# Optimization experiments

Measured on AMD Instinct MI355X. Metric: run time of the kernel, lower is better.

The kernel has to match this reference:

```python
import jax, jax.numpy as jnp
import numpy as np

T, B, IN_DIM, HID, ACT = 512, 256, 256, 256, 16


def _dense_params(key, din, dout, scale=0.02):
    kw, _ = jax.random.split(key)
    return jax.random.normal(kw, (din, dout), jnp.float32) * scale, jnp.zeros((dout,), jnp.float32)


def setup_inputs() -> dict:
    key = jax.random.key(0)
    ks = jax.random.split(key, 12)
    x = jax.random.normal(ks[0], (T, B, IN_DIM), jnp.float32)
    dones = jax.random.bernoulli(ks[1], 0.05, (T, B))
    h0_c = jnp.zeros((B, HID), jnp.float32)
    h0_h = jnp.zeros((B, HID), jnp.float32)
    W_embed, b_embed = _dense_params(ks[2], IN_DIM, HID)
    # OptimizedLSTMCell: fused gate projections, gate order (i, f, g, o)
    Wi = jax.random.normal(ks[3], (HID, 4 * HID), jnp.float32) * 0.02
    Wh = jax.random.normal(ks[4], (HID, 4 * HID), jnp.float32) * 0.02
    b_lstm = jnp.zeros((4 * HID,), jnp.float32)
    Wa1, ba1 = _dense_params(ks[5], HID, HID // 2)
    Wa2, ba2 = _dense_params(ks[6], HID // 2, HID // 2)
    Wa3, ba3 = _dense_params(ks[7], HID // 2, ACT, scale=0.01)
    Wc1, bc1 = _dense_params(ks[8], HID, HID // 2)
    Wc2, bc2 = _dense_params(ks[9], HID // 2, HID // 2)
    Wc3, bc3 = _dense_params(ks[10], HID // 2, 1)
    return dict(x=x, dones=dones, h0_c=h0_c, h0_h=h0_h,
                W_embed=W_embed, b_embed=b_embed, Wi=Wi, Wh=Wh, b_lstm=b_lstm,
                Wa1=Wa1, ba1=ba1, Wa2=Wa2, ba2=ba2, Wa3=Wa3, ba3=ba3,
                Wc1=Wc1, bc1=bc1, Wc2=Wc2, bc2=bc2, Wc3=Wc3, bc3=bc3)


def reference(x, dones, h0_c, h0_h, W_embed, b_embed, Wi, Wh, b_lstm,
              Wa1, ba1, Wa2, ba2, Wa3, ba3, Wc1, bc1, Wc2, bc2, Wc3, bc3):
    # embed (note: source overwrites first Dense; effective embed is one Dense+relu)
    embed = jax.nn.relu(jnp.einsum('tbi,ih->tbh', x, W_embed) + b_embed)

    def step(carry, inp):
        c, h = carry
        xt, rt = inp  # xt: [B, HID], rt: [B] bool
        m = rt[:, None]
        c = jnp.where(m, 0.0, c)  # reset_carry is zeros (initialize_carry)
        h = jnp.where(m, 0.0, h)
        z = xt @ Wi + h @ Wh + b_lstm  # [B, 4*HID]
        i, f, g, o = jnp.split(z, 4, axis=-1)
        c_new = jax.nn.sigmoid(f) * c + jax.nn.sigmoid(i) * jnp.tanh(g)
        h_new = jax.nn.sigmoid(o) * jnp.tanh(c_new)
        return (c_new, h_new), h_new

    (c_fin, h_fin), hs = jax.lax.scan(step, (h0_c, h0_h), (embed, dones))

    a = jnp.tanh(jnp.einsum('tbh,hk->tbk', hs, Wa1) + ba1)
    a = jnp.tanh(a @ Wa2 + ba2)
    logits = a @ Wa3 + ba3  # [T, B, ACT]

    v = jnp.tanh(jnp.einsum('tbh,hk->tbk', hs, Wc1) + bc1)
    v = jnp.tanh(v @ Wc2 + bc2)
    value = jnp.squeeze(v @ Wc3 + bc3, axis=-1)  # [T, B]

    return c_fin, h_fin, logits, value
```

## Files before the change

kernel.cpp:

```cpp
#include <hip/hip_runtime.h>
#include <stdint.h>


typedef short v8s __attribute__((ext_vector_type(8)));
typedef float v4f __attribute__((ext_vector_type(4)));

#define DEV static __device__ __forceinline__
#define DT_THRESH 4096

DEV float b2f(unsigned short h) {
    union { unsigned int u; float f; } v; v.u = ((unsigned int)h) << 16; return v.f;
}
DEV unsigned short f2b(float f) {
    union { float f; unsigned int u; } v; v.f = f;
    unsigned int u = v.u;
    return (unsigned short)((u + 0x7fffu + ((u >> 16) & 1u)) >> 16);
}
DEV float sigf(float x) {
    x = fminf(fmaxf(x, -30.f), 30.f);
    return 1.f / (1.f + __expf(-x));
}
DEV float tanh_(float x) {
    x = fminf(fmaxf(x, -15.f), 15.f);
    float e = __expf(-2.f * x);
    return (1.f - e) / (1.f + e);
}

__global__ __launch_bounds__(1024) void dones_k(const void* __restrict__ raw,
                                                int* __restrict__ dst,
                                                int* __restrict__ dt) {
    __shared__ int bad_int, bad_bf;
    int tid = threadIdx.x;
    if (tid == 0) { bad_int = 0; bad_bf = 0; dt[0] = 0; }
    __syncthreads();
    const unsigned int* w = (const unsigned int*)raw;
    int li = 0, lb = 0;
    for (int i = tid; i < 32768; i += 1024) {
        unsigned int v = w[i];
        if (v > 1u) li = 1;
        unsigned int h0 = v & 0xffffu, h1 = v >> 16;
        if ((h0 != 0u && h0 != 0x3f80u) || (h1 != 0u && h1 != 0x3f80u)) lb = 1;
    }
    if (li) atomicOr(&bad_int, 1);
    if (lb) atomicOr(&bad_bf, 1);
    __syncthreads();
    int mode = (!bad_int) ? 0 : ((!bad_bf) ? 1 : 2);
    for (int e = tid; e < 131072; e += 1024) {
        int v;
        if (mode == 0)      v = (((const int*)raw)[e] != 0);
        else if (mode == 1) v = (((const unsigned short*)raw)[e] != 0);
        else                v = (((const unsigned char*)raw)[e] != 0);
        dst[e] = v;
    }
}

__global__ __launch_bounds__(256) void detect_k(const unsigned short* __restrict__ xr,
                                                int* __restrict__ dt) {
    int tid = blockIdx.x * 256 + threadIdx.x;
    int cnt = 0;
    for (int i = tid; i < (1 << 24); i += 16384) {
        unsigned int e = (xr[i] >> 7) & 0xffu;
        cnt += (e >= 140u);
    }
    for (int o = 32; o; o >>= 1) cnt += __shfl_down(cnt, o);
    if ((threadIdx.x & 63) == 0 && cnt) atomicAdd(dt, cnt);
}

__global__ __launch_bounds__(256) void cvt_x_k(const void* __restrict__ xr,
                                               unsigned short* __restrict__ xb,
                                               const int* __restrict__ dt) {
    int fp32i = dt[0] > DT_THRESH;
    long i4 = (long)blockIdx.x * 256 + threadIdx.x;
    if (fp32i) {
        float4 v = ((const float4*)xr)[i4];
        uint2 p;
        p.x = (unsigned int)f2b(v.x) | ((unsigned int)f2b(v.y) << 16);
        p.y = (unsigned int)f2b(v.z) | ((unsigned int)f2b(v.w) << 16);
        ((uint2*)xb)[i4] = p;
    } else {
        ((uint2*)xb)[i4] = ((const uint2*)xr)[i4];
    }
}

struct TransArgs {
    const void* src[9];
    unsigned short* dst[9];
    int R[9];
    int C[9];
    int prefix[10];
    int total;
};

__global__ __launch_bounds__(256) void trans_kernel(TransArgs a, const int* __restrict__ dt) {
    int fp32i = dt[0] > DT_THRESH;
    int id = blockIdx.x * 256 + threadIdx.x;
    if (id >= a.total) return;
    int m = 0;
#pragma unroll
    for (int k = 0; k < 9; k++)
        if (id >= a.prefix[k + 1]) m = k + 1;
    int e = id - a.prefix[m];
    int C = a.C[m];
    int r = e / C, c = e % C;
    unsigned short v;
    if (fp32i) v = f2b(((const float*)a.src[m])[e]);
    else       v = ((const unsigned short*)a.src[m])[e];
    a.dst[m][c * a.R[m] + r] = v;
}

template <int TN, int ACT, int OM>
__global__ __launch_bounds__(256) void gemm_k(const unsigned short* __restrict__ A,
                                              const unsigned short* __restrict__ BT,
                                              const unsigned short* __restrict__ bias,
                                              void* __restrict__ Cout, long coff,
                                              const int* __restrict__ dtf,
                                              int N, int K) {
    __shared__ unsigned short As[128][40];
    __shared__ unsigned short Bs[TN][40];
    const int tid = threadIdx.x;
    const int l = tid & 63, w = tid >> 6;
    const long m0 = (long)blockIdx.x * 128;
    const int n0 = blockIdx.y * TN;
    constexpr int NRT = (TN == 128) ? 4 : 2;
    constexpr int NCT = (TN == 128) ? 4 : 1;
    int fp32o = (OM == 1) ? (dtf[0] > DT_THRESH) : 0;

    v4f acc[NRT][NCT];
    for (int i = 0; i < NRT; i++)
        for (int j = 0; j < NCT; j++) acc[i][j] = v4f{0.f, 0.f, 0.f, 0.f};

    for (int kc = 0; kc < K; kc += 32) {
        {
            int row = tid >> 1, part = tid & 1;
            const uint4* src = (const uint4*)(A + (m0 + row) * K + kc + part * 16);
            uint4 v0 = src[0], v1 = src[1];
            *(uint4*)&As[row][part * 16] = v0;
            *(uint4*)&As[row][part * 16 + 8] = v1;
        }
        if (TN == 128) {
            int row = tid >> 1, part = tid & 1;
            const uint4* src = (const uint4*)(BT + (long)(n0 + row) * K + kc + part * 16);
            uint4 v0 = src[0], v1 = src[1];
            *(uint4*)&Bs[row][part * 16] = v0;
            *(uint4*)&Bs[row][part * 16 + 8] = v1;
        } else if (tid < 32) {
            int row = tid >> 1, part = tid & 1;
            const uint4* src = (const uint4*)(BT + (long)(n0 + row) * K + kc + part * 16);
            uint4 v0 = src[0], v1 = src[1];
            *(uint4*)&Bs[row][part * 16] = v0;
            *(uint4*)&Bs[row][part * 16 + 8] = v1;
        }
        __syncthreads();

        v8s af[NRT], bf[NCT];
#pragma unroll
        for (int i = 0; i < NRT; i++) {
            int rt = (TN == 128) ? ((w >> 1) * 4 + i) : (w * 2 + i);
            af[i] = *(const v8s*)&As[rt * 16 + (l & 15)][(l >> 4) * 8];
        }
#pragma unroll
        for (int j = 0; j < NCT; j++) {
            int ct = (TN == 128) ? ((w & 1) * 4 + j) : 0;
            bf[j] = *(const v8s*)&Bs[ct * 16 + (l & 15)][(l >> 4) * 8];
        }
#pragma unroll
        for (int i = 0; i < NRT; i++)
#pragma unroll
            for (int j = 0; j < NCT; j++)
                acc[i][j] = __builtin_amdgcn_mfma_f32_16x16x32_bf16(af[i], bf[j], acc[i][j], 0, 0, 0);
        __syncthreads();
    }

#pragma unroll
    for (int j = 0; j < NCT; j++) {
        int ct = (TN == 128) ? ((w & 1) * 4 + j) : 0;
        int col = ct * 16 + (l & 15);
        float bv = b2f(bias[n0 + col]);
#pragma unroll
        for (int i = 0; i < NRT; i++) {
            int rt = (TN == 128) ? ((w >> 1) * 4 + i) : (w * 2 + i);
#pragma unroll
            for (int q = 0; q < 4; q++) {
                long row = m0 + rt * 16 + (l >> 4) * 4 + q;
                float v = acc[i][j][q] + bv;
                if (ACT == 1) v = fmaxf(v, 0.f);
                if (ACT == 2) v = tanh_(v);
                long idx = coff + row * (long)N + n0 + col;
                if (OM == 1 && fp32o) ((float*)Cout)[idx] = v;
                else ((unsigned short*)Cout)[idx] = f2b(v);
            }
        }
    }
}

#define HB_WORDS 65536

__global__ __launch_bounds__(64) void lstm_k(const unsigned short* __restrict__ xz,
                                             const int* __restrict__ dones,
                                             const void* __restrict__ h0c,
                                             const void* __restrict__ h0h,
                                             const unsigned short* __restrict__ WhT,
                                             unsigned int* __restrict__ hb,
                                             unsigned short* __restrict__ hs,
                                             void* __restrict__ outv,
                                             const int* __restrict__ dtf) {
    __shared__ unsigned short Whs[64][264];
    __shared__ unsigned short hlds[16][264];
    __shared__ unsigned short xzs[16][72];
    __shared__ int dns[16];

    const int l = threadIdx.x;
    const int cluster = blockIdx.x & 15;
    const int rank = blockIdx.x >> 4;
    const int bt = cluster * 16;
    const int m = l & 15;
    const int qq = l >> 4;
    const int hc = rank * 16 + m;
    const int fp32o = dtf[0] > DT_THRESH;
    const int meven = ((m & 1) == 0);

    {
        int zc = qq * 256 + rank * 16 + m;
        const unsigned short* srcp = WhT + (long)zc * 256;
#pragma unroll
        for (int k8 = 0; k8 < 32; k8++) {
            uint4 v = *(const uint4*)(srcp + k8 * 8);
            *(uint4*)&Whs[l][k8 * 8] = v;
        }
    }
    __syncthreads();

    float c[4], hn[4];
#pragma unroll
    for (int q = 0; q < 4; q++) {
        int row = qq * 4 + q;
        long idx = (long)(bt + row) * 256 + hc;
        c[q] = fp32o ? ((const float*)h0c)[idx] : b2f(((const unsigned short*)h0c)[idx]);
        float h0 = fp32o ? ((const float*)h0h)[idx] : b2f(((const unsigned short*)h0h)[idx]);
        unsigned short hbits = f2b(h0);
        __hip_atomic_store(&hb[(size_t)cluster * 4096 + row * 256 + hc],
                           (unsigned int)hbits,
                           __ATOMIC_RELAXED, __HIP_MEMORY_SCOPE_AGENT);
        hn[q] = 0.f;
    }

    int dead = 0;
    unsigned int va[64];

    for (int t = 0; t < 512; t++) {
        const unsigned int tag = (unsigned int)t;
        const unsigned int* rb = hb + (size_t)(t & 1) * HB_WORDS + (size_t)cluster * 4096;

        if (l < 16) dns[l] = dones[t * 256 + bt + l];
        {
            int row = l >> 2, g = l & 3;
            const uint4* src = (const uint4*)(xz + ((long)(t * 256 + bt + row)) * 1024 + g * 256 + rank * 16);
            uint4 v0 = src[0], v1 = src[1];
            *(uint4*)&xzs[row][g * 16] = v0;
            *(uint4*)&xzs[row][g * 16 + 8] = v1;
        }

        if (!dead) {
            int guard = 0;
            while (true) {
#pragma unroll
                for (int i = 0; i < 64; i++)
                    va[i] = __hip_atomic_load(&rb[i * 64 + l],
                                              __ATOMIC_RELAXED, __HIP_MEMORY_SCOPE_AGENT);
                unsigned int okl = 1u;
#pragma unroll
                for (int i = 0; i < 64; i++) okl &= ((va[i] >> 16) == tag) ? 1u : 0u;
                if (__ballot(okl != 0u) == ~0ull) break;
                if (++guard > (1 << 13)) { dead = 1; break; }
            }
        }

#pragma unroll
        for (int i = 0; i < 64; i++)
            hlds[i >> 2][(i & 3) * 64 + l] = (unsigned short)(va[i] & 0xffffu);
        __syncthreads();

        int dnA = dns[m];
        v4f acc[4];
#pragma unroll
        for (int g = 0; g < 4; g++) acc[g] = v4f{0.f, 0.f, 0.f, 0.f};
#pragma unroll
        for (int ks = 0; ks < 8; ks++) {
            v8s a = *(const v8s*)&hlds[m][ks * 32 + qq * 8];
            if (dnA) a = v8s{0, 0, 0, 0, 0, 0, 0, 0};
#pragma unroll
            for (int g = 0; g < 4; g++) {
                v8s b = *(const v8s*)&Whs[g * 16 + m][ks * 32 + qq * 8];
                acc[g] = __builtin_amdgcn_mfma_f32_16x16x32_bf16(a, b, acc[g], 0, 0, 0);
            }
        }

        unsigned int* wb = hb + (size_t)((t + 1) & 1) * HB_WORDS + (size_t)cluster * 4096;
#pragma unroll
        for (int q = 0; q < 4; q++) {
            int row = qq * 4 + q;
            float zi = acc[0][q] + b2f(xzs[row][0 + m]);
            float zf = acc[1][q] + b2f(xzs[row][16 + m]);
            float zg = acc[2][q] + b2f(xzs[row][32 + m]);
            float zo = acc[3][q] + b2f(xzs[row][48 + m]);
            float cm = dns[row] ? 0.f : c[q];
            float cn = sigf(zf) * cm + sigf(zi) * tanh_(zg);
            float h = sigf(zo) * tanh_(cn);
            c[q] = cn;
            hn[q] = h;
            unsigned short hbits = f2b(h);
            __hip_atomic_store(&wb[row * 256 + hc],
                               (((unsigned int)(t + 1)) << 16) | (unsigned int)hbits,
                               __ATOMIC_RELAXED, __HIP_MEMORY_SCOPE_AGENT);
            unsigned int pr = (unsigned int)__shfl_xor((int)hbits, 1);
            if (meven) {
                unsigned int wv = (unsigned int)hbits | (pr << 16);
                ((unsigned int*)hs)[((long)(t * 256 + bt + row)) * 128 + rank * 8 + (m >> 1)] = wv;
            }
        }
        __syncthreads();
    }

#pragma unroll
    for (int q = 0; q < 4; q++) {
        int row = qq * 4 + q;
        long i1 = (long)(bt + row) * 256 + hc;
        long i2 = 65536 + i1;
        if (fp32o) {
            ((float*)outv)[i1] = c[q];
            ((float*)outv)[i2] = hn[q];
        } else {
            ((unsigned short*)outv)[i1] = f2b(c[q]);
            ((unsigned short*)outv)[i2] = f2b(hn[q]);
        }
    }
}

__global__ __launch_bounds__(256) void value_k(const unsigned short* __restrict__ V2,
                                               const unsigned short* __restrict__ Wc3T,
                                               const unsigned short* __restrict__ bc3,
                                               void* __restrict__ outv,
                                               const int* __restrict__ dtf) {
    int tid = threadIdx.x;
    int l = tid & 63, w = tid >> 6;
    int fp32o = dtf[0] > DT_THRESH;
    long row = (long)blockIdx.x * 32 + w * 8 + (l >> 3);
    int sub = l & 7;
    const unsigned short* vp = V2 + row * 128 + sub * 16;
    float s = 0.f;
#pragma unroll
    for (int j = 0; j < 16; j++) s += b2f(vp[j]) * b2f(Wc3T[sub * 16 + j]);
    s += __shfl_xor(s, 1);
    s += __shfl_xor(s, 2);
    s += __shfl_xor(s, 4);
    if (sub == 0) {
        float v = s + b2f(bc3[0]);
        if (fp32o) ((float*)outv)[2228224 + row] = v;
        else ((unsigned short*)outv)[2228224 + row] = f2b(v);
    }
}

extern "C" void kernel_launch(void* const* d_in, const int* in_sizes, int n_in,
                              void* d_out, int out_size, void* d_ws, size_t ws_size,
                              hipStream_t stream) {
    const void* x             = d_in[0];
    const void* dones_raw     = d_in[1];
    const void* h0c           = d_in[2];
    const void* h0h           = d_in[3];
    const void* We  = d_in[4];
    const unsigned short* be  = (const unsigned short*)d_in[5];
    const void* Wi  = d_in[6];
    const void* Wh  = d_in[7];
    const unsigned short* bl  = (const unsigned short*)d_in[8];
    const void* Wa1 = d_in[9];
    const unsigned short* ba1 = (const unsigned short*)d_in[10];
    const void* Wa2 = d_in[11];
    const unsigned short* ba2 = (const unsigned short*)d_in[12];
    const void* Wa3 = d_in[13];
    const unsigned short* ba3 = (const unsigned short*)d_in[14];
    const void* Wc1 = d_in[15];
    const unsigned short* bc1 = (const unsigned short*)d_in[16];
    const void* Wc2 = d_in[17];
    const unsigned short* bc2 = (const unsigned short*)d_in[18];
    const void* Wc3 = d_in[19];
    const unsigned short* bc3 = (const unsigned short*)d_in[20];
    char* ws = (char*)d_ws;

    unsigned short* WeT  = (unsigned short*)(ws + 0);
    unsigned short* WiT  = (unsigned short*)(ws + 131072);
    unsigned short* WhT  = (unsigned short*)(ws + 655360);
    unsigned short* Wa1T = (unsigned short*)(ws + 1179648);
    unsigned short* Wa2T = (unsigned short*)(ws + 1245184);
    unsigned short* Wa3T = (unsigned short*)(ws + 1277952);
    unsigned short* Wc1T = (unsigned short*)(ws + 1282048);
    unsigned short* Wc2T = (unsigned short*)(ws + 1347584);
    unsigned short* Wc3T = (unsigned short*)(ws + 1380352);
    int*            DT   = (int*)(ws + 1380608);
    unsigned int*   HB   = (unsigned int*)(ws + 1380672);
    int*            DN   = (int*)(ws + 1904960);
    unsigned short* XB   = (unsigned short*)(ws + 2429248);
    unsigned short* E    = (unsigned short*)(ws + 69538112);
    unsigned short* XZ   = (unsigned short*)(ws + 136646976);
    unsigned short* HS   = (unsigned short*)(ws + 405082432);
    unsigned short* H1   = XB;
    unsigned short* H2   = XB + 16777216;

    TransArgs ta;
    {
        const void* srcs[9] = {We, Wi, Wh, Wa1, Wa2, Wa3, Wc1, Wc2, Wc3};
        unsigned short* dsts[9] = {WeT, WiT, WhT, Wa1T, Wa2T, Wa3T, Wc1T, Wc2T, Wc3T};
        int Rs[9] = {256, 256, 256, 256, 128, 128, 256, 128, 128};
        int Cs[9] = {256, 1024, 1024, 128, 128, 16, 128, 128, 1};
        int p = 0;
        for (int i = 0; i < 9; i++) {
            ta.src[i] = srcs[i];
            ta.dst[i] = dsts[i];
            ta.R[i] = Rs[i];
            ta.C[i] = Cs[i];
            ta.prefix[i] = p;
            p += Rs[i] * Cs[i];
        }
        ta.prefix[9] = p;
        ta.total = p;
    }

    dones_k<<<1, 1024, 0, stream>>>(dones_raw, DN, DT);
    detect_k<<<64, 256, 0, stream>>>((const unsigned short*)x, DT);
    cvt_x_k<<<32768, 256, 0, stream>>>(x, XB, DT);
    trans_kernel<<<2697, 256, 0, stream>>>(ta, DT);

    gemm_k<128, 1, 0><<<dim3(1024, 2), 256, 0, stream>>>(XB, WeT, be, E, 0, nullptr, 256, 256);
    gemm_k<128, 0, 0><<<dim3(1024, 8), 256, 0, stream>>>(E, WiT, bl, XZ, 0, nullptr, 1024, 256);
    lstm_k<<<256, 64, 0, stream>>>(XZ, DN, h0c, h0h, WhT, HB, HS, d_out, DT);
    gemm_k<128, 2, 0><<<dim3(1024, 1), 256, 0, stream>>>(HS, Wa1T, ba1, H1, 0, nullptr, 128, 256);
    gemm_k<128, 2, 0><<<dim3(1024, 1), 256, 0, stream>>>(H1, Wa2T, ba2, H2, 0, nullptr, 128, 128);
    gemm_k<16, 0, 1><<<dim3(1024, 1), 256, 0, stream>>>(H2, Wa3T, ba3, d_out, 131072, DT, 16, 128);
    gemm_k<128, 2, 0><<<dim3(1024, 1), 256, 0, stream>>>(HS, Wc1T, bc1, H1, 0, nullptr, 128, 256);
    gemm_k<128, 2, 0><<<dim3(1024, 1), 256, 0, stream>>>(H1, Wc2T, bc2, H2, 0, nullptr, 128, 128);
    value_k<<<4096, 256, 0, stream>>>(H2, Wc3T, bc3, d_out, DT);
}
```

Baseline: 2.841 ms.

## Restructure LSTM recurrence into 32 blocks of 512 threads with register-resident Wh

The recurrent kernel moves from 256 single-wave blocks, where 16 blocks cooperate per batch cluster, to 32 blocks of 8 waves where only 2 blocks share a cluster. Each block now covers 128 hidden units, so it owns half of h locally and only polls its partner's half through global memory. Wh fragments are kept in registers instead of LDS, and gate pre-activations are exchanged through an LDS buffer with an extra barrier. The aim is to cut the cross-block spin-wait and global traffic per timestep. In exchange it adds register pressure, an intra-block reduction step, and uses far fewer CUs.

```diff
diff --git a/kernel.cpp b/kernel.cpp
--- a/kernel.cpp
+++ b/kernel.cpp
@@ -195,143 +195,155 @@
 
 #define HB_WORDS 65536
 
-__global__ __launch_bounds__(64) void lstm_k(const unsigned short* __restrict__ xz,
-                                             const int* __restrict__ dones,
-                                             const void* __restrict__ h0c,
-                                             const void* __restrict__ h0h,
-                                             const unsigned short* __restrict__ WhT,
-                                             unsigned int* __restrict__ hb,
-                                             unsigned short* __restrict__ hs,
-                                             void* __restrict__ outv,
-                                             const int* __restrict__ dtf) {
-    __shared__ unsigned short Whs[64][264];
-    __shared__ unsigned short hlds[16][264];
-    __shared__ unsigned short xzs[16][72];
-    __shared__ int dns[16];
-
-    const int l = threadIdx.x;
+__global__ __launch_bounds__(512, 2) void lstm_k(const unsigned short* __restrict__ xz,
+                                                 const int* __restrict__ dones,
+                                                 const void* __restrict__ h0c,
+                                                 const void* __restrict__ h0h,
+                                                 const unsigned short* __restrict__ WhT,
+                                                 unsigned int* __restrict__ hb,
+                                                 unsigned short* __restrict__ hs,
+                                                 void* __restrict__ outv,
+                                                 const int* __restrict__ dtf) {
+    __shared__ unsigned short hlds[16][256];
+    __shared__ float zlds[4][16][132];
+
+    const int tid = threadIdx.x;
+    const int l = tid & 63;
+    const int w = tid >> 6;
     const int cluster = blockIdx.x & 15;
-    const int rank = blockIdx.x >> 4;
+    const int r = blockIdx.x >> 4;
+    const int p = r ^ 1;
     const int bt = cluster * 16;
-    const int m = l & 15;
-    const int qq = l >> 4;
-    const int hc = rank * 16 + m;
     const int fp32o = dtf[0] > DT_THRESH;
-    const int meven = ((m & 1) == 0);
-
-    {
-        int zc = qq * 256 + rank * 16 + m;
-        const unsigned short* srcp = WhT + (long)zc * 256;
-#pragma unroll
-        for (int k8 = 0; k8 < 32; k8++) {
-            uint4 v = *(const uint4*)(srcp + k8 * 8);
-            *(uint4*)&Whs[l][k8 * 8] = v;
-        }
-    }
-    __syncthreads();
-
-    float c[4], hn[4];
-#pragma unroll
-    for (int q = 0; q < 4; q++) {
-        int row = qq * 4 + q;
-        long idx = (long)(bt + row) * 256 + hc;
-        c[q] = fp32o ? ((const float*)h0c)[idx] : b2f(((const unsigned short*)h0c)[idx]);
+    const int gate = w & 3;
+    const int hblk = (w >> 2) * 64;
+    const int l15 = l & 15;
+    const int lq = l >> 4;
+
+    v8s bw[4][8];
+#pragma unroll
+    for (int j = 0; j < 4; j++) {
+        const unsigned short* wp =
+            WhT + (long)(gate * 256 + r * 128 + hblk + j * 16 + l15) * 256 + lq * 8;
+#pragma unroll
+        for (int ks = 0; ks < 8; ks++) bw[j][ks] = *(const v8s*)(wp + ks * 32);
+    }
+
+    float c[4], hcur[4] = {0.f, 0.f, 0.f, 0.f};
+#pragma unroll
+    for (int i = 0; i < 4; i++) {
+        int cell = i * 512 + tid;
+        int row = cell >> 7, hid = cell & 127;
+        long idx = (long)(bt + row) * 256 + r * 128 + hid;
+        c[i] = fp32o ? ((const float*)h0c)[idx] : b2f(((const unsigned short*)h0c)[idx]);
         float h0 = fp32o ? ((const float*)h0h)[idx] : b2f(((const unsigned short*)h0h)[idx]);
         unsigned short hbits = f2b(h0);
-        __hip_atomic_store(&hb[(size_t)cluster * 4096 + row * 256 + hc],
+        hlds[row][(r * 128 + hid) ^ ((row & 7) * 8)] = hbits;
+        __hip_atomic_store(&hb[(size_t)cluster * 4096 + row * 256 + r * 128 + hid],
                            (unsigned int)hbits,
                            __ATOMIC_RELAXED, __HIP_MEMORY_SCOPE_AGENT);
-        hn[q] = 0.f;
     }
 
     int dead = 0;
-    unsigned int va[64];
+    unsigned int va[4] = {0u, 0u, 0u, 0u};
 
     for (int t = 0; t < 512; t++) {
+        unsigned short xzp[16];
+#pragma unroll
+        for (int j = 0; j < 4; j++)
+#pragma unroll
+            for (int q = 0; q < 4; q++)
+                xzp[j * 4 + q] = xz[(long)(t * 256 + bt + lq * 4 + q) * 1024 +
+                                    (gate * 256 + r * 128 + hblk + j * 16 + l15)];
+        int dn_a = dones[t * 256 + bt + l15];
+        int dn_c[4];
+#pragma unroll
+        for (int i = 0; i < 4; i++) dn_c[i] = dones[t * 256 + bt + i * 4 + (tid >> 7)];
+
         const unsigned int tag = (unsigned int)t;
         const unsigned int* rb = hb + (size_t)(t & 1) * HB_WORDS + (size_t)cluster * 4096;
-
-        if (l < 16) dns[l] = dones[t * 256 + bt + l];
-        {
-            int row = l >> 2, g = l & 3;
-            const uint4* src = (const uint4*)(xz + ((long)(t * 256 + bt + row)) * 1024 + g * 256 + rank * 16);
-            uint4 v0 = src[0], v1 = src[1];
-            *(uint4*)&xzs[row][g * 16] = v0;
-            *(uint4*)&xzs[row][g * 16 + 8] = v1;
-        }
-
         if (!dead) {
             int guard = 0;
             while (true) {
 #pragma unroll
-                for (int i = 0; i < 64; i++)
-                    va[i] = __hip_atomic_load(&rb[i * 64 + l],
+                for (int i = 0; i < 4; i++) {
+                    int cell = i * 512 + tid;
+                    va[i] = __hip_atomic_load(&rb[(cell >> 7) * 256 + p * 128 + (cell & 127)],
                                               __ATOMIC_RELAXED, __HIP_MEMORY_SCOPE_AGENT);
-                unsigned int okl = 1u;
-#pragma unroll
-                for (int i = 0; i < 64; i++) okl &= ((va[i] >> 16) == tag) ? 1u : 0u;
+                }
+                unsigned int okl = ((va[0] >> 16) == tag) & ((va[1] >> 16) == tag) &
+                                   ((va[2] >> 16) == tag) & ((va[3] >> 16) == tag);
                 if (__ballot(okl != 0u) == ~0ull) break;
                 if (++guard > (1 << 13)) { dead = 1; break; }
             }
         }
-
-#pragma unroll
-        for (int i = 0; i < 64; i++)
-            hlds[i >> 2][(i & 3) * 64 + l] = (unsigned short)(va[i] & 0xffffu);
+#pragma unroll
+        for (int i = 0; i < 4; i++) {
+            int cell = i * 512 + tid;
+            int row = cell >> 7, hid = cell & 127;
+            hlds[row][(p * 128 + hid) ^ ((row & 7) * 8)] = (unsigned short)(va[i] & 0xffffu);
+        }
         __syncthreads();
 
-        int dnA = dns[m];
         v4f acc[4];
 #pragma unroll
-        for (int g = 0; g < 4; g++) acc[g] = v4f{0.f, 0.f, 0.f, 0.f};
+        for (int j = 0; j < 4; j++)
+#pragma unroll
+            for (int q = 0; q < 4; q++) acc[j][q] = b2f(xzp[j * 4 + q]);
 #pragma unroll
         for (int ks = 0; ks < 8; ks++) {
-            v8s a = *(const v8s*)&hlds[m][ks * 32 + qq * 8];
-            if (dnA) a = v8s{0, 0, 0, 0, 0, 0, 0, 0};
-#pragma unroll
-            for (int g = 0; g < 4; g++) {
-                v8s b = *(const v8s*)&Whs[g * 16 + m][ks * 32 + qq * 8];
-                acc[g] = __builtin_amdgcn_mfma_f32_16x16x32_bf16(a, b, acc[g], 0, 0, 0);
-            }
-        }
+            v8s a = *(const v8s*)&hlds[l15][(ks * 32 + lq * 8) ^ ((l15 & 7) * 8)];
+            if (dn_a) a = v8s{0, 0, 0, 0, 0, 0, 0, 0};
+#pragma unroll
+            for (int j = 0; j < 4; j++)
+                acc[j] = __builtin_amdgcn_mfma_f32_16x16x32_bf16(a, bw[j][ks], acc[j], 0, 0, 0);
+        }
+#pragma unroll
+        for (int j = 0; j < 4; j++)
+#pragma unroll
+            for (int q = 0; q < 4; q++)
+                zlds[gate][lq * 4 + q][hblk + j * 16 + l15] = acc[j][q];
+        __syncthreads();
 
         unsigned int* wb = hb + (size_t)((t + 1) & 1) * HB_WORDS + (size_t)cluster * 4096;
 #pragma unroll
-        for (int q = 0; q < 4; q++) {
-            int row = qq * 4 + q;
-            float zi = acc[0][q] + b2f(xzs[row][0 + m]);
-            float zf = acc[1][q] + b2f(xzs[row][16 + m]);
-            float zg = acc[2][q] + b2f(xzs[row][32 + m]);
-            float zo = acc[3][q] + b2f(xzs[row][48 + m]);
-            float cm = dns[row] ? 0.f : c[q];
+        for (int i = 0; i < 4; i++) {
+            int cell = i * 512 + tid;
+            int row = cell >> 7, hid = cell & 127;
+            float zi = zlds[0][row][hid];
+            float zf = zlds[1][row][hid];
+            float zg = zlds[2][row][hid];
+            float zo = zlds[3][row][hid];
+            float cm = dn_c[i] ? 0.f : c[i];
             float cn = sigf(zf) * cm + sigf(zi) * tanh_(zg);
             float h = sigf(zo) * tanh_(cn);
-            c[q] = cn;
-            hn[q] = h;
+            c[i] = cn;
+            hcur[i] = h;
             unsigned short hbits = f2b(h);
-            __hip_atomic_store(&wb[row * 256 + hc],
+            hlds[row][(r * 128 + hid) ^ ((row & 7) * 8)] = hbits;
+            __hip_atomic_store(&wb[row * 256 + r * 128 + hid],
                                (((unsigned int)(t + 1)) << 16) | (unsigned int)hbits,
                                __ATOMIC_RELAXED, __HIP_MEMORY_SCOPE_AGENT);
             unsigned int pr = (unsigned int)__shfl_xor((int)hbits, 1);
-            if (meven) {
+            if ((tid & 1) == 0) {
                 unsigned int wv = (unsigned int)hbits | (pr << 16);
-                ((unsigned int*)hs)[((long)(t * 256 + bt + row)) * 128 + rank * 8 + (m >> 1)] = wv;
+                ((unsigned int*)hs)[((long)(t * 256 + bt + row)) * 128 + ((r * 128 + hid) >> 1)] = wv;
             }
         }
-        __syncthreads();
-    }
-
-#pragma unroll
-    for (int q = 0; q < 4; q++) {
-        int row = qq * 4 + q;
-        long i1 = (long)(bt + row) * 256 + hc;
+    }
+
+#pragma unroll
+    for (int i = 0; i < 4; i++) {
+        int cell = i * 512 + tid;
+        int row = cell >> 7, hid = cell & 127;
+        long i1 = (long)(bt + row) * 256 + r * 128 + hid;
         long i2 = 65536 + i1;
         if (fp32o) {
-            ((float*)outv)[i1] = c[q];
-            ((float*)outv)[i2] = hn[q];
+            ((float*)outv)[i1] = c[i];
+            ((float*)outv)[i2] = hcur[i];
         } else {
-            ((unsigned short*)outv)[i1] = f2b(c[q]);
-            ((unsigned short*)outv)[i2] = f2b(hn[q]);
+            ((unsigned short*)outv)[i1] = f2b(c[i]);
+            ((unsigned short*)outv)[i2] = f2b(hcur[i]);
         }
     }
 }
@@ -431,7 +443,7 @@
 
     gemm_k<128, 1, 0><<<dim3(1024, 2), 256, 0, stream>>>(XB, WeT, be, E, 0, nullptr, 256, 256);
     gemm_k<128, 0, 0><<<dim3(1024, 8), 256, 0, stream>>>(E, WiT, bl, XZ, 0, nullptr, 1024, 256);
-    lstm_k<<<256, 64, 0, stream>>>(XZ, DN, h0c, h0h, WhT, HB, HS, d_out, DT);
+    lstm_k<<<32, 512, 0, stream>>>(XZ, DN, h0c, h0h, WhT, HB, HS, d_out, DT);
     gemm_k<128, 2, 0><<<dim3(1024, 1), 256, 0, stream>>>(HS, Wa1T, ba1, H1, 0, nullptr, 128, 256);
     gemm_k<128, 2, 0><<<dim3(1024, 1), 256, 0, stream>>>(H1, Wa2T, ba2, H2, 0, nullptr, 128, 128);
     gemm_k<16, 0, 1><<<dim3(1024, 1), 256, 0, stream>>>(H2, Wa3T, ba3, d_out, 131072, DT, 16, 128);
```

Measured after the change: 2.657 ms. -6.5%, faster.

## Run each LSTM batch cluster in one 1024-thread block with LDS-exchanged hidden state

Applied to the files above, without the earlier changes.

The LSTM recurrence no longer spreads each 16-row batch cluster across 16 single-wave blocks that trade hidden state through tagged global atomics and spin-polling. Each cluster now runs in one 1024-thread block (16 waves), swaps h through double-buffered, XOR-swizzled LDS, and synchronises with __syncthreads. The recurrent weights are streamed from global/L2 each step with register double-buffering instead of being held in LDS. The next step's xz and dones are prefetched into registers, the xz values seed the accumulator, and reset masking is applied when h is written. This removes cross-block global round trips and polling per step, at the cost of rereading Wh from cache every step and using only 16 workgroups.

```diff
diff --git a/kernel.cpp b/kernel.cpp
--- a/kernel.cpp
+++ b/kernel.cpp
@@ -193,145 +193,130 @@
     }
 }
 
-#define HB_WORDS 65536
-
-__global__ __launch_bounds__(64) void lstm_k(const unsigned short* __restrict__ xz,
-                                             const int* __restrict__ dones,
-                                             const void* __restrict__ h0c,
-                                             const void* __restrict__ h0h,
-                                             const unsigned short* __restrict__ WhT,
-                                             unsigned int* __restrict__ hb,
-                                             unsigned short* __restrict__ hs,
-                                             void* __restrict__ outv,
-                                             const int* __restrict__ dtf) {
-    __shared__ unsigned short Whs[64][264];
-    __shared__ unsigned short hlds[16][264];
-    __shared__ unsigned short xzs[16][72];
-    __shared__ int dns[16];
-
-    const int l = threadIdx.x;
-    const int cluster = blockIdx.x & 15;
-    const int rank = blockIdx.x >> 4;
+__global__ __launch_bounds__(1024, 4) void lstm_k(const unsigned short* __restrict__ xz,
+                                                  const int* __restrict__ dones,
+                                                  const void* __restrict__ h0c,
+                                                  const void* __restrict__ h0h,
+                                                  const unsigned short* __restrict__ WhT,
+                                                  unsigned short* __restrict__ hs,
+                                                  void* __restrict__ outv,
+                                                  const int* __restrict__ dtf) {
+    __shared__ unsigned short hlds[2][16][256];
+
+    const int tid = threadIdx.x;
+    const int l = tid & 63;
+    const int w = tid >> 6;
+    const int cluster = blockIdx.x;
     const int bt = cluster * 16;
-    const int m = l & 15;
-    const int qq = l >> 4;
-    const int hc = rank * 16 + m;
     const int fp32o = dtf[0] > DT_THRESH;
-    const int meven = ((m & 1) == 0);
-
-    {
-        int zc = qq * 256 + rank * 16 + m;
-        const unsigned short* srcp = WhT + (long)zc * 256;
-#pragma unroll
-        for (int k8 = 0; k8 < 32; k8++) {
-            uint4 v = *(const uint4*)(srcp + k8 * 8);
-            *(uint4*)&Whs[l][k8 * 8] = v;
-        }
-    }
-    __syncthreads();
-
-    float c[4], hn[4];
+    const int l15 = l & 15;
+    const int lq = l >> 4;
+    const int hid = w * 16 + l15;
+
+    const unsigned short* bp[4];
+#pragma unroll
+    for (int g = 0; g < 4; g++)
+        bp[g] = WhT + (long)(g * 256 + hid) * 256 + lq * 8;
+
+    float c[4], hcur[4] = {0.f, 0.f, 0.f, 0.f};
+    int dn_cur[4], dn_nxt[4];
+    unsigned short xzb[16];
 #pragma unroll
     for (int q = 0; q < 4; q++) {
-        int row = qq * 4 + q;
-        long idx = (long)(bt + row) * 256 + hc;
+        int row = lq * 4 + q;
+        long idx = (long)(bt + row) * 256 + hid;
         c[q] = fp32o ? ((const float*)h0c)[idx] : b2f(((const unsigned short*)h0c)[idx]);
         float h0 = fp32o ? ((const float*)h0h)[idx] : b2f(((const unsigned short*)h0h)[idx]);
-        unsigned short hbits = f2b(h0);
-        __hip_atomic_store(&hb[(size_t)cluster * 4096 + row * 256 + hc],
-                           (unsigned int)hbits,
-                           __ATOMIC_RELAXED, __HIP_MEMORY_SCOPE_AGENT);
-        hn[q] = 0.f;
-    }
-
-    int dead = 0;
-    unsigned int va[64];
+        dn_cur[q] = dones[bt + row];
+        dn_nxt[q] = dones[256 + bt + row];
+        hlds[0][row][hid ^ ((row & 7) * 8)] = dn_cur[q] ? (unsigned short)0 : f2b(h0);
+    }
+#pragma unroll
+    for (int g = 0; g < 4; g++)
+#pragma unroll
+        for (int q = 0; q < 4; q++)
+            xzb[g * 4 + q] = xz[(long)(bt + lq * 4 + q) * 1024 + g * 256 + hid];
+    __syncthreads();
 
     for (int t = 0; t < 512; t++) {
-        const unsigned int tag = (unsigned int)t;
-        const unsigned int* rb = hb + (size_t)(t & 1) * HB_WORDS + (size_t)cluster * 4096;
-
-        if (l < 16) dns[l] = dones[t * 256 + bt + l];
+        const int cur = t & 1, nxt = cur ^ 1;
+
+        v4f acc[4];
+#pragma unroll
+        for (int g = 0; g < 4; g++)
+#pragma unroll
+            for (int q = 0; q < 4; q++) acc[g][q] = b2f(xzb[g * 4 + q]);
+
         {
-            int row = l >> 2, g = l & 3;
-            const uint4* src = (const uint4*)(xz + ((long)(t * 256 + bt + row)) * 1024 + g * 256 + rank * 16);
-            uint4 v0 = src[0], v1 = src[1];
-            *(uint4*)&xzs[row][g * 16] = v0;
-            *(uint4*)&xzs[row][g * 16 + 8] = v1;
-        }
-
-        if (!dead) {
-            int guard = 0;
-            while (true) {
-#pragma unroll
-                for (int i = 0; i < 64; i++)
-                    va[i] = __hip_atomic_load(&rb[i * 64 + l],
-                                              __ATOMIC_RELAXED, __HIP_MEMORY_SCOPE_AGENT);
-                unsigned int okl = 1u;
-#pragma unroll
-                for (int i = 0; i < 64; i++) okl &= ((va[i] >> 16) == tag) ? 1u : 0u;
-                if (__ballot(okl != 0u) == ~0ull) break;
-                if (++guard > (1 << 13)) { dead = 1; break; }
+            int tn = (t < 511) ? t + 1 : t;
+#pragma unroll
+            for (int g = 0; g < 4; g++)
+#pragma unroll
+                for (int q = 0; q < 4; q++)
+                    xzb[g * 4 + q] = xz[(long)(tn * 256 + bt + lq * 4 + q) * 1024 + g * 256 + hid];
+        }
+
+        v8s bb0[4], bb1[4];
+#pragma unroll
+        for (int g = 0; g < 4; g++) bb0[g] = *(const v8s*)(bp[g]);
+#pragma unroll
+        for (int ks = 0; ks < 8; ks++) {
+            v8s a = *(const v8s*)&hlds[cur][l15][(ks * 32 + lq * 8) ^ ((l15 & 7) * 8)];
+            if (ks + 1 < 8) {
+#pragma unroll
+                for (int g = 0; g < 4; g++) {
+                    v8s nb = *(const v8s*)(bp[g] + (ks + 1) * 32);
+                    if ((ks & 1) == 0) bb1[g] = nb; else bb0[g] = nb;
+                }
             }
-        }
-
-#pragma unroll
-        for (int i = 0; i < 64; i++)
-            hlds[i >> 2][(i & 3) * 64 + l] = (unsigned short)(va[i] & 0xffffu);
-        __syncthreads();
-
-        int dnA = dns[m];
-        v4f acc[4];
-#pragma unroll
-        for (int g = 0; g < 4; g++) acc[g] = v4f{0.f, 0.f, 0.f, 0.f};
-#pragma unroll
-        for (int ks = 0; ks < 8; ks++) {
-            v8s a = *(const v8s*)&hlds[m][ks * 32 + qq * 8];
-            if (dnA) a = v8s{0, 0, 0, 0, 0, 0, 0, 0};
 #pragma unroll
             for (int g = 0; g < 4; g++) {
-                v8s b = *(const v8s*)&Whs[g * 16 + m][ks * 32 + qq * 8];
-                acc[g] = __builtin_amdgcn_mfma_f32_16x16x32_bf16(a, b, acc[g], 0, 0, 0);
+                v8s bfr = ((ks & 1) == 0) ? bb0[g] : bb1[g];
+                acc[g] = __builtin_amdgcn_mfma_f32_16x16x32_bf16(a, bfr, acc[g], 0, 0, 0);
             }
         }
 
-        unsigned int* wb = hb + (size_t)((t + 1) & 1) * HB_WORDS + (size_t)cluster * 4096;
 #pragma unroll
         for (int q = 0; q < 4; q++) {
-            int row = qq * 4 + q;
-            float zi = acc[0][q] + b2f(xzs[row][0 + m]);
-            float zf = acc[1][q] + b2f(xzs[row][16 + m]);
-            float zg = acc[2][q] + b2f(xzs[row][32 + m]);
-            float zo = acc[3][q] + b2f(xzs[row][48 + m]);
-            float cm = dns[row] ? 0.f : c[q];
+            int row = lq * 4 + q;
+            float zi = acc[0][q];
+            float zf = acc[1][q];
+            float zg = acc[2][q];
+            float zo = acc[3][q];
+            float cm = dn_cur[q] ? 0.f : c[q];
             float cn = sigf(zf) * cm + sigf(zi) * tanh_(zg);
             float h = sigf(zo) * tanh_(cn);
             c[q] = cn;
-            hn[q] = h;
+            hcur[q] = h;
             unsigned short hbits = f2b(h);
-            __hip_atomic_store(&wb[row * 256 + hc],
-                               (((unsigned int)(t + 1)) << 16) | (unsigned int)hbits,
-                               __ATOMIC_RELAXED, __HIP_MEMORY_SCOPE_AGENT);
+            hlds[nxt][row][hid ^ ((row & 7) * 8)] = dn_nxt[q] ? (unsigned short)0 : hbits;
             unsigned int pr = (unsigned int)__shfl_xor((int)hbits, 1);
-            if (meven) {
-                unsigned int wv = (unsigned int)hbits | (pr << 16);
-                ((unsigned int*)hs)[((long)(t * 256 + bt + row)) * 128 + rank * 8 + (m >> 1)] = wv;
+            if ((l & 1) == 0) {
+                ((unsigned int*)hs)[((long)(t * 256 + bt + row)) * 128 + (hid >> 1)] =
+                    (unsigned int)hbits | (pr << 16);
             }
         }
+#pragma unroll
+        for (int q = 0; q < 4; q++) dn_cur[q] = dn_nxt[q];
+        {
+            int tn2 = (t + 2 < 512) ? t + 2 : 511;
+#pragma unroll
+            for (int q = 0; q < 4; q++) dn_nxt[q] = dones[tn2 * 256 + bt + lq * 4 + q];
+        }
         __syncthreads();
     }
 
 #pragma unroll
     for (int q = 0; q < 4; q++) {
-        int row = qq * 4 + q;
-        long i1 = (long)(bt + row) * 256 + hc;
+        int row = lq * 4 + q;
+        long i1 = (long)(bt + row) * 256 + hid;
         long i2 = 65536 + i1;
         if (fp32o) {
             ((float*)outv)[i1] = c[q];
-            ((float*)outv)[i2] = hn[q];
+            ((float*)outv)[i2] = hcur[q];
         } else {
             ((unsigned short*)outv)[i1] = f2b(c[q]);
-            ((unsigned short*)outv)[i2] = f2b(hn[q]);
+            ((unsigned short*)outv)[i2] = f2b(hcur[q]);
         }
     }
 }
@@ -404,6 +389,7 @@
     unsigned short* HS   = (unsigned short*)(ws + 405082432);
     unsigned short* H1   = XB;
     unsigned short* H2   = XB + 16777216;
+    (void)HB;
 
     TransArgs ta;
     {
@@ -431,7 +417,7 @@
 
     gemm_k<128, 1, 0><<<dim3(1024, 2), 256, 0, stream>>>(XB, WeT, be, E, 0, nullptr, 256, 256);
     gemm_k<128, 0, 0><<<dim3(1024, 8), 256, 0, stream>>>(E, WiT, bl, XZ, 0, nullptr, 1024, 256);
-    lstm_k<<<256, 64, 0, stream>>>(XZ, DN, h0c, h0h, WhT, HB, HS, d_out, DT);
+    lstm_k<<<16, 1024, 0, stream>>>(XZ, DN, h0c, h0h, WhT, HS, d_out, DT);
     gemm_k<128, 2, 0><<<dim3(1024, 1), 256, 0, stream>>>(HS, Wa1T, ba1, H1, 0, nullptr, 128, 256);
     gemm_k<128, 2, 0><<<dim3(1024, 1), 256, 0, stream>>>(H1, Wa2T, ba2, H2, 0, nullptr, 128, 128);
     gemm_k<16, 0, 1><<<dim3(1024, 1), 256, 0, stream>>>(H2, Wa3T, ba3, d_out, 131072, DT, 16, 128);
```

Result: slower. 6.287 ms (+121.3%).
